# Optimization experiments

Measured on AMD Instinct MI355X. Metric: run time of the kernel, lower is better.

## Reference

```python
import jax, jax.numpy as jnp
import numpy as np

N_NODES = 200000
IN_DIM = 128
HID = 256
OUT = 128
B = 2048
K = 16  # sampled temporal fanout per hop


def setup_inputs() -> dict:
    rng = np.random.default_rng(0)
    x = rng.standard_normal((N_NODES, IN_DIM), dtype=np.float32)
    batch = rng.integers(0, N_NODES, size=B).astype(np.int32)
    ts = rng.uniform(0.5, 1.0, size=B).astype(np.float32)

    # hop 1: K temporal neighbors per seed node, edge times <= query time
    nbr1 = rng.integers(0, N_NODES, size=B * K).astype(np.int32)
    t_edge1 = (rng.uniform(0.0, 1.0, size=(B, K)) * ts[:, None]).astype(np.float32)
    n_times1 = t_edge1.max(axis=1)                       # [B] max neighbor time per seed
    seg1 = np.repeat(np.arange(B, dtype=np.int32), K)    # [E1]

    # second-level frontier: neighbors first, then the batch itself
    nodes2 = np.concatenate([nbr1, batch])               # [N2 = B*K + B]
    t2 = np.concatenate([t_edge1.reshape(-1), ts]).astype(np.float32)
    N2 = nodes2.shape[0]

    # hop 2
    nbr2 = rng.integers(0, N_NODES, size=N2 * K).astype(np.int32)
    t_edge2 = (rng.uniform(0.0, 1.0, size=(N2, K)) * t2[:, None]).astype(np.float32)
    n_times2 = t_edge2.max(axis=1)                       # [N2]
    seg2 = np.repeat(np.arange(N2, dtype=np.int32), K)   # [E2]

    def lin(ko, fan_out, fan_in):
        lim = 1.0 / np.sqrt(fan_in)
        kw, kb = jax.random.split(ko)
        W = jax.random.uniform(kw, (fan_out, fan_in), jnp.float32, -lim, lim)
        b = jax.random.uniform(kb, (fan_out,), jnp.float32, -lim, lim)
        return W, b

    key = jax.random.key(0)
    k1, k2, k3, k4, k5 = jax.random.split(key, 5)
    W1n, b1n = lin(k1, HID, IN_DIM)
    W1h, b1h = lin(k2, HID, IN_DIM)
    W2n, b2n = lin(k3, OUT, HID)
    W2h, b2h = lin(k4, OUT, HID)
    t_kernel = jax.random.uniform(k5, (1,), jnp.float32)

    return {
        "x": jnp.asarray(x), "ts": jnp.asarray(ts), "t2": jnp.asarray(t2),
        "n_times1": jnp.asarray(n_times1), "n_times2": jnp.asarray(n_times2),
        "W1n": W1n, "b1n": b1n, "W1h": W1h, "b1h": b1h,
        "W2n": W2n, "b2n": b2n, "W2h": W2h, "b2h": b2h,
        "t_kernel": t_kernel,
        "nodes2": jnp.asarray(nodes2), "nbr2": jnp.asarray(nbr2),
        "seg2": jnp.asarray(seg2), "seg1": jnp.asarray(seg1),
    }


def reference(x, ts, t2, n_times1, n_times2, W1n, b1n, W1h, b1h,
              W2n, b2n, W2h, b2h, t_kernel, nodes2, nbr2, seg2, seg1):
    N2 = nodes2.shape[0]
    Bn = ts.shape[0]
    E1 = N2 - Bn

    def decay(dt):  # exp(-t_kernel * dt), t_kernel shape (1,) broadcasts
        return jnp.exp(-t_kernel * dt)

    # ---- layer 1 (inner recursion; layer-0 embeddings are raw features x) ----
    agg2 = jax.ops.segment_sum(x[nbr2], seg2, num_segments=N2)   # [N2, D] neighbor sums
    hn1 = x[nodes2] * decay(t2 - n_times2)[:, None]              # self feats * temporal decay
    h1 = jax.nn.relu(agg2 @ W1n.T + b1n + hn1 @ W1h.T + b1h)     # [N2, HID]

    # ---- layer 2 (top) ----
    agg1 = jax.ops.segment_sum(h1[:E1], seg1, num_segments=Bn)   # [B, HID]
    hn2 = h1[E1:] * decay(ts - n_times1)[:, None]                # [B, HID]
    out = jax.nn.relu(agg1 @ W2n.T + b2n + hn2 @ W2h.T + b2h)    # [B, OUT]
    return out
```

## Files before the change

kernel.cpp:

```cpp
#include <hip/hip_runtime.h>
#include <hip/hip_bf16.h>

#define N2V    34816
#define BATCH  2048
#define E1V    32768
#define KFAN   16
#define INDIM  128
#define HID    256
#define OUTD   128

#define OFF_BS1   0
#define OFF_BS2   256
#define OFF_WC1B  384
#define OFF_WC2B  33152
#define OFF_AGG1B 65920
#define OFF_H1S   328064

typedef __attribute__((ext_vector_type(8))) short bf16x8;
typedef __attribute__((ext_vector_type(4))) short short4v;
typedef __attribute__((ext_vector_type(4))) float f32x4;

__device__ __forceinline__ float bf2f(short u) {
  union { unsigned u32; float f; } cv;
  cv.u32 = ((unsigned)(unsigned short)u) << 16;
  return cv.f;
}

__device__ __forceinline__ short f2b(float f) {
  __hip_bfloat16 h = __float2bfloat16(f);
  return *reinterpret_cast<short*>(&h);
}

__global__ __launch_bounds__(256) void prepack_kernel(
    const float* __restrict__ W1n, const float* __restrict__ b1n,
    const float* __restrict__ W1h, const float* __restrict__ b1h,
    const float* __restrict__ W2n, const float* __restrict__ b2n,
    const float* __restrict__ W2h, const float* __restrict__ b2h,
    __hip_bfloat16* __restrict__ Wc1b, __hip_bfloat16* __restrict__ Wc2b,
    float* __restrict__ bs1, float* __restrict__ bs2) {
  int idx = blockIdx.x * 256 + threadIdx.x;
  int j1 = idx >> 8, c1 = idx & 255;
  float v1 = (c1 < 128) ? W1n[j1 * 128 + c1] : W1h[j1 * 128 + (c1 - 128)];
  Wc1b[idx] = __float2bfloat16(v1);
  int j2 = idx >> 9, c2 = idx & 511;
  float v2 = (c2 < 256) ? W2n[j2 * 256 + c2] : W2h[j2 * 256 + (c2 - 256)];
  Wc2b[idx] = __float2bfloat16(v2);
  if (idx < 256) bs1[idx] = b1n[idx] + b1h[idx];
  if (idx < 128) bs2[idx] = b2n[idx] + b2h[idx];
}

__global__ __launch_bounds__(256) void fused1_kernel(
    const float* __restrict__ x, const float* __restrict__ t2,
    const float* __restrict__ n_times2, const int* __restrict__ nodes2,
    const int* __restrict__ nbr2, const float* __restrict__ tk,
    const __hip_bfloat16* __restrict__ Wc1b, const float* __restrict__ bs1,
    __hip_bfloat16* __restrict__ agg1b, __hip_bfloat16* __restrict__ h1s) {
  __shared__ __hip_bfloat16 z[16][264];
  const int t = threadIdx.x;
  const int i0 = blockIdx.x * 16;
  {
    const int r = t >> 4;
    const int c = t & 15;
    const int i = i0 + r;
    const float4* __restrict__ x4 = (const float4*)x;

    const int4* nb4 = reinterpret_cast<const int4*>(nbr2) + i * 4;
    int4 n0 = nb4[0], n1 = nb4[1], n2 = nb4[2], n3 = nb4[3];
    const int idx[16] = {n0.x, n0.y, n0.z, n0.w, n1.x, n1.y, n1.z, n1.w,
                         n2.x, n2.y, n2.z, n2.w, n3.x, n3.y, n3.z, n3.w};

    float4 s0 = {0.f, 0.f, 0.f, 0.f};
    float4 s1 = {0.f, 0.f, 0.f, 0.f};
#pragma unroll
    for (int k = 0; k < KFAN; ++k) {
      const float4* rp = x4 + (size_t)idx[k] * 32;
      float4 v0 = rp[c];
      float4 v1 = rp[16 + c];
      s0.x += v0.x; s0.y += v0.y; s0.z += v0.z; s0.w += v0.w;
      s1.x += v1.x; s1.y += v1.y; s1.z += v1.z; s1.w += v1.w;
    }
    const float dec = __expf(-tk[0] * (t2[i] - n_times2[i]));
    const float4* sp = x4 + (size_t)nodes2[i] * 32;
    float4 u0 = sp[c];
    float4 u1 = sp[16 + c];

    char* zrow = (char*)&z[0][0] + r * 528;
    short4v p;
    p = (short4v){f2b(s0.x), f2b(s0.y), f2b(s0.z), f2b(s0.w)};
    *reinterpret_cast<short4v*>(zrow + c * 8) = p;
    p = (short4v){f2b(s1.x), f2b(s1.y), f2b(s1.z), f2b(s1.w)};
    *reinterpret_cast<short4v*>(zrow + 128 + c * 8) = p;
    p = (short4v){f2b(u0.x * dec), f2b(u0.y * dec), f2b(u0.z * dec), f2b(u0.w * dec)};
    *reinterpret_cast<short4v*>(zrow + 256 + c * 8) = p;
    p = (short4v){f2b(u1.x * dec), f2b(u1.y * dec), f2b(u1.z * dec), f2b(u1.w * dec)};
    *reinterpret_cast<short4v*>(zrow + 384 + c * 8) = p;
  }
  __syncthreads();

  const int wid = t >> 6;
  const int lane = t & 63;
  const int lr = lane & 15;
  const int lk8 = (lane >> 4) * 8;
  const int ncol0 = wid * 64;
  const short* __restrict__ wsrc = (const short*)Wc1b;

  f32x4 acc[4];
#pragma unroll
  for (int n = 0; n < 4; ++n) acc[n] = (f32x4){0.f, 0.f, 0.f, 0.f};

#pragma unroll
  for (int ks = 0; ks < 8; ++ks) {
    const int kb = ks * 32 + lk8;
    bf16x8 a = *reinterpret_cast<const bf16x8*>((char*)&z[0][0] + lr * 528 + kb * 2);
#pragma unroll
    for (int nt = 0; nt < 4; ++nt) {
      bf16x8 b = *reinterpret_cast<const bf16x8*>(
          wsrc + (size_t)(ncol0 + nt * 16 + lr) * 256 + kb);
      acc[nt] = __builtin_amdgcn_mfma_f32_16x16x32_bf16(a, b, acc[nt], 0, 0, 0);
    }
  }

  if (i0 < E1V) {
#pragma unroll
    for (int nt = 0; nt < 4; ++nt) {
      const int col = ncol0 + nt * 16 + lr;
      const float bias = bs1[col];
      float v = 0.f;
#pragma unroll
      for (int q = 0; q < 4; ++q) v += fmaxf(acc[nt][q] + bias, 0.f);
      v += __shfl_xor(v, 16);
      v += __shfl_xor(v, 32);
      if (lane < 16) {
        agg1b[(size_t)blockIdx.x * HID + col] = __float2bfloat16(v);
      }
    }
  } else {
    const int orow = (lane >> 4) * 4;
#pragma unroll
    for (int nt = 0; nt < 4; ++nt) {
      const int col = ncol0 + nt * 16 + lr;
      const float bias = bs1[col];
#pragma unroll
      for (int q = 0; q < 4; ++q) {
        const int row = i0 - E1V + orow + q;
        h1s[(size_t)row * HID + col] =
            __float2bfloat16(fmaxf(acc[nt][q] + bias, 0.f));
      }
    }
  }
}

__global__ __launch_bounds__(64) void layer2_kernel(
    const __hip_bfloat16* __restrict__ agg1b, const __hip_bfloat16* __restrict__ h1s,
    const float* __restrict__ ts, const float* __restrict__ n_times1,
    const float* __restrict__ tk, const __hip_bfloat16* __restrict__ Wc2b,
    const float* __restrict__ bs2, float* __restrict__ out) {
  const int lane = threadIdx.x;
  const int b0 = blockIdx.x * 16;
  const int lr = lane & 15;
  const int lk8 = (lane >> 4) * 8;
  const int row = b0 + lr;

  const float dec = __expf(-tk[0] * (ts[row] - n_times1[row]));
  const short* __restrict__ ag = (const short*)agg1b;
  const short* __restrict__ hs = (const short*)h1s;
  const short* __restrict__ w2 = (const short*)Wc2b;

  f32x4 acc[8];
#pragma unroll
  for (int n = 0; n < 8; ++n) acc[n] = (f32x4){0.f, 0.f, 0.f, 0.f};

#pragma unroll
  for (int ks = 0; ks < 16; ++ks) {
    const int kb = ks * 32 + lk8;
    bf16x8 a;
    if (kb < HID) {
      a = *reinterpret_cast<const bf16x8*>(ag + (size_t)row * HID + kb);
    } else {
      bf16x8 hv = *reinterpret_cast<const bf16x8*>(hs + (size_t)row * HID + (kb - HID));
#pragma unroll
      for (int e = 0; e < 8; ++e) a[e] = f2b(bf2f(hv[e]) * dec);
    }
#pragma unroll
    for (int nt = 0; nt < 8; ++nt) {
      bf16x8 b = *reinterpret_cast<const bf16x8*>(
          w2 + (size_t)(nt * 16 + lr) * 512 + kb);
      acc[nt] = __builtin_amdgcn_mfma_f32_16x16x32_bf16(a, b, acc[nt], 0, 0, 0);
    }
  }

  const int orow = (lane >> 4) * 4;
#pragma unroll
  for (int nt = 0; nt < 8; ++nt) {
    const int col = nt * 16 + lr;
    const float bias = bs2[col];
#pragma unroll
    for (int q = 0; q < 4; ++q) {
      out[(size_t)(b0 + orow + q) * OUTD + col] = fmaxf(acc[nt][q] + bias, 0.f);
    }
  }
}

extern "C" void kernel_launch(void* const* d_in, const int* in_sizes, int n_in,
                              void* d_out, int out_size, void* d_ws, size_t ws_size,
                              hipStream_t stream) {
  const float* x        = (const float*)d_in[0];
  const float* ts       = (const float*)d_in[1];
  const float* t2       = (const float*)d_in[2];
  const float* n_times1 = (const float*)d_in[3];
  const float* n_times2 = (const float*)d_in[4];
  const float* W1n      = (const float*)d_in[5];
  const float* b1n      = (const float*)d_in[6];
  const float* W1h      = (const float*)d_in[7];
  const float* b1h      = (const float*)d_in[8];
  const float* W2n      = (const float*)d_in[9];
  const float* b2n      = (const float*)d_in[10];
  const float* W2h      = (const float*)d_in[11];
  const float* b2h      = (const float*)d_in[12];
  const float* tk       = (const float*)d_in[13];
  const int*   nodes2   = (const int*)d_in[14];
  const int*   nbr2     = (const int*)d_in[15];

  float* ws = (float*)d_ws;
  float* bs1 = ws + OFF_BS1;
  float* bs2 = ws + OFF_BS2;
  __hip_bfloat16* Wc1b  = (__hip_bfloat16*)(ws + OFF_WC1B);
  __hip_bfloat16* Wc2b  = (__hip_bfloat16*)(ws + OFF_WC2B);
  __hip_bfloat16* agg1b = (__hip_bfloat16*)(ws + OFF_AGG1B);
  __hip_bfloat16* h1s   = (__hip_bfloat16*)(ws + OFF_H1S);
  float* out = (float*)d_out;

  prepack_kernel<<<256, 256, 0, stream>>>(W1n, b1n, W1h, b1h,
                                          W2n, b2n, W2h, b2h,
                                          Wc1b, Wc2b, bs1, bs2);
  fused1_kernel<<<N2V / 16, 256, 0, stream>>>(x, t2, n_times2, nodes2, nbr2, tk,
                                              Wc1b, bs1, agg1b, h1s);
  layer2_kernel<<<BATCH / 16, 64, 0, stream>>>(agg1b, h1s, ts, n_times1, tk,
                                               Wc2b, bs2, out);
}
```

Measured before the change: 77.21 us.

## Process two row tiles per block, overlapping next tile's gather with current GEMM

Each fused1 block now handles two 16-row tiles with a double-buffered LDS staging area. The gather loads for the second tile (first half of the features plus the self row) are issued before the first tile's MFMA GEMM so memory latency can overlap compute, with explicit barriers and scheduling fences around it. The grid is halved and launch bounds request 3 blocks per CU. In exchange, register pressure rises (16 float4 values held across the GEMM), which could lower occupancy or cause spills, and halving the block count reduces parallelism for a gather-bound kernel.

```diff
diff --git a/kernel.cpp b/kernel.cpp
--- a/kernel.cpp
+++ b/kernel.cpp
@@ -8,6 +8,7 @@
 #define INDIM  128
 #define HID    256
 #define OUTD   128
+#define E1TILES (E1V / 16)
 
 #define OFF_BS1   0
 #define OFF_BS2   256
@@ -49,26 +50,86 @@
   if (idx < 128) bs2[idx] = b2n[idx] + b2h[idx];
 }
 
-__global__ __launch_bounds__(256) void fused1_kernel(
+__device__ __forceinline__ void gemm_tile(
+    const __hip_bfloat16* zb, int tile, int t,
+    const short* __restrict__ wsrc, const float* __restrict__ bs1,
+    __hip_bfloat16* __restrict__ agg1b, __hip_bfloat16* __restrict__ h1s) {
+  const int wid = t >> 6;
+  const int lane = t & 63;
+  const int lr = lane & 15;
+  const int lk8 = (lane >> 4) * 8;
+  const int ncol0 = wid * 64;
+
+  f32x4 acc[4];
+#pragma unroll
+  for (int n = 0; n < 4; ++n) acc[n] = (f32x4){0.f, 0.f, 0.f, 0.f};
+
+#pragma unroll
+  for (int ks = 0; ks < 8; ++ks) {
+    const int kb = ks * 32 + lk8;
+    bf16x8 a = *reinterpret_cast<const bf16x8*>(
+        (const char*)zb + lr * 528 + kb * 2);
+#pragma unroll
+    for (int nt = 0; nt < 4; ++nt) {
+      bf16x8 b = *reinterpret_cast<const bf16x8*>(
+          wsrc + (size_t)(ncol0 + nt * 16 + lr) * 256 + kb);
+      acc[nt] = __builtin_amdgcn_mfma_f32_16x16x32_bf16(a, b, acc[nt], 0, 0, 0);
+    }
+  }
+
+  if (tile < E1TILES) {
+#pragma unroll
+    for (int nt = 0; nt < 4; ++nt) {
+      const int col = ncol0 + nt * 16 + lr;
+      const float bias = bs1[col];
+      float v = 0.f;
+#pragma unroll
+      for (int q = 0; q < 4; ++q) v += fmaxf(acc[nt][q] + bias, 0.f);
+      v += __shfl_xor(v, 16);
+      v += __shfl_xor(v, 32);
+      if (lane < 16) {
+        agg1b[(size_t)tile * HID + col] = __float2bfloat16(v);
+      }
+    }
+  } else {
+    const int orow = (lane >> 4) * 4;
+    const int rbase = tile * 16 - E1V;
+#pragma unroll
+    for (int nt = 0; nt < 4; ++nt) {
+      const int col = ncol0 + nt * 16 + lr;
+      const float bias = bs1[col];
+#pragma unroll
+      for (int q = 0; q < 4; ++q) {
+        h1s[(size_t)(rbase + orow + q) * HID + col] =
+            __float2bfloat16(fmaxf(acc[nt][q] + bias, 0.f));
+      }
+    }
+  }
+}
+
+__global__ __launch_bounds__(256, 3) void fused1_kernel(
     const float* __restrict__ x, const float* __restrict__ t2,
     const float* __restrict__ n_times2, const int* __restrict__ nodes2,
     const int* __restrict__ nbr2, const float* __restrict__ tk,
     const __hip_bfloat16* __restrict__ Wc1b, const float* __restrict__ bs1,
     __hip_bfloat16* __restrict__ agg1b, __hip_bfloat16* __restrict__ h1s) {
-  __shared__ __hip_bfloat16 z[16][264];
+  __shared__ __hip_bfloat16 z[2][16][264];
   const int t = threadIdx.x;
-  const int i0 = blockIdx.x * 16;
+  const int r = t >> 4;
+  const int c = t & 15;
+  const int tileA = blockIdx.x * 2;
+  const int tileB = tileA + 1;
+  const int iA = tileA * 16 + r;
+  const int iB = tileB * 16 + r;
+  const float4* __restrict__ x4 = (const float4*)x;
+  const float tkv = tk[0];
+  const short* __restrict__ wsrc = (const short*)Wc1b;
+
   {
-    const int r = t >> 4;
-    const int c = t & 15;
-    const int i = i0 + r;
-    const float4* __restrict__ x4 = (const float4*)x;
-
-    const int4* nb4 = reinterpret_cast<const int4*>(nbr2) + i * 4;
+    const int4* nb4 = reinterpret_cast<const int4*>(nbr2) + iA * 4;
     int4 n0 = nb4[0], n1 = nb4[1], n2 = nb4[2], n3 = nb4[3];
     const int idx[16] = {n0.x, n0.y, n0.z, n0.w, n1.x, n1.y, n1.z, n1.w,
                          n2.x, n2.y, n2.z, n2.w, n3.x, n3.y, n3.z, n3.w};
-
     float4 s0 = {0.f, 0.f, 0.f, 0.f};
     float4 s1 = {0.f, 0.f, 0.f, 0.f};
 #pragma unroll
@@ -79,12 +140,12 @@
       s0.x += v0.x; s0.y += v0.y; s0.z += v0.z; s0.w += v0.w;
       s1.x += v1.x; s1.y += v1.y; s1.z += v1.z; s1.w += v1.w;
     }
-    const float dec = __expf(-tk[0] * (t2[i] - n_times2[i]));
-    const float4* sp = x4 + (size_t)nodes2[i] * 32;
+    const float dec = __expf(-tkv * (t2[iA] - n_times2[iA]));
+    const float4* sp = x4 + (size_t)nodes2[iA] * 32;
     float4 u0 = sp[c];
     float4 u1 = sp[16 + c];
 
-    char* zrow = (char*)&z[0][0] + r * 528;
+    char* zrow = (char*)&z[0][0][0] + r * 528;
     short4v p;
     p = (short4v){f2b(s0.x), f2b(s0.y), f2b(s0.z), f2b(s0.w)};
     *reinterpret_cast<short4v*>(zrow + c * 8) = p;
@@ -95,59 +156,61 @@
     p = (short4v){f2b(u1.x * dec), f2b(u1.y * dec), f2b(u1.z * dec), f2b(u1.w * dec)};
     *reinterpret_cast<short4v*>(zrow + 384 + c * 8) = p;
   }
-  __syncthreads();
-
-  const int wid = t >> 6;
-  const int lane = t & 63;
-  const int lr = lane & 15;
-  const int lk8 = (lane >> 4) * 8;
-  const int ncol0 = wid * 64;
-  const short* __restrict__ wsrc = (const short*)Wc1b;
-
-  f32x4 acc[4];
-#pragma unroll
-  for (int n = 0; n < 4; ++n) acc[n] = (f32x4){0.f, 0.f, 0.f, 0.f};
-
-#pragma unroll
-  for (int ks = 0; ks < 8; ++ks) {
-    const int kb = ks * 32 + lk8;
-    bf16x8 a = *reinterpret_cast<const bf16x8*>((char*)&z[0][0] + lr * 528 + kb * 2);
-#pragma unroll
-    for (int nt = 0; nt < 4; ++nt) {
-      bf16x8 b = *reinterpret_cast<const bf16x8*>(
-          wsrc + (size_t)(ncol0 + nt * 16 + lr) * 256 + kb);
-      acc[nt] = __builtin_amdgcn_mfma_f32_16x16x32_bf16(a, b, acc[nt], 0, 0, 0);
-    }
-  }
-
-  if (i0 < E1V) {
-#pragma unroll
-    for (int nt = 0; nt < 4; ++nt) {
-      const int col = ncol0 + nt * 16 + lr;
-      const float bias = bs1[col];
-      float v = 0.f;
-#pragma unroll
-      for (int q = 0; q < 4; ++q) v += fmaxf(acc[nt][q] + bias, 0.f);
-      v += __shfl_xor(v, 16);
-      v += __shfl_xor(v, 32);
-      if (lane < 16) {
-        agg1b[(size_t)blockIdx.x * HID + col] = __float2bfloat16(v);
-      }
-    }
-  } else {
-    const int orow = (lane >> 4) * 4;
-#pragma unroll
-    for (int nt = 0; nt < 4; ++nt) {
-      const int col = ncol0 + nt * 16 + lr;
-      const float bias = bs1[col];
-#pragma unroll
-      for (int q = 0; q < 4; ++q) {
-        const int row = i0 - E1V + orow + q;
-        h1s[(size_t)row * HID + col] =
-            __float2bfloat16(fmaxf(acc[nt][q] + bias, 0.f));
-      }
-    }
-  }
+
+  int idxB[16];
+  {
+    const int4* nb4 = reinterpret_cast<const int4*>(nbr2) + iB * 4;
+    int4 n0 = nb4[0], n1 = nb4[1], n2 = nb4[2], n3 = nb4[3];
+    idxB[0] = n0.x; idxB[1] = n0.y; idxB[2]  = n0.z; idxB[3]  = n0.w;
+    idxB[4] = n1.x; idxB[5] = n1.y; idxB[6]  = n1.z; idxB[7]  = n1.w;
+    idxB[8] = n2.x; idxB[9] = n2.y; idxB[10] = n2.z; idxB[11] = n2.w;
+    idxB[12] = n3.x; idxB[13] = n3.y; idxB[14] = n3.z; idxB[15] = n3.w;
+  }
+  float4 vB[16];
+#pragma unroll
+  for (int k = 0; k < KFAN; ++k)
+    vB[k] = x4[(size_t)idxB[k] * 32 + c];
+  const float4* spB = x4 + (size_t)nodes2[iB] * 32;
+  float4 uB0 = spB[c];
+  float4 uB1 = spB[16 + c];
+  const float decB = __expf(-tkv * (t2[iB] - n_times2[iB]));
+
+  asm volatile("s_waitcnt lgkmcnt(0)" ::: "memory");
+  __builtin_amdgcn_s_barrier();
+  __builtin_amdgcn_sched_barrier(0);
+
+  gemm_tile(&z[0][0][0], tileA, t, wsrc, bs1, agg1b, h1s);
+
+  {
+    float4 s0 = {0.f, 0.f, 0.f, 0.f};
+#pragma unroll
+    for (int k = 0; k < KFAN; ++k) {
+      s0.x += vB[k].x; s0.y += vB[k].y; s0.z += vB[k].z; s0.w += vB[k].w;
+    }
+    float4 s1 = {0.f, 0.f, 0.f, 0.f};
+#pragma unroll
+    for (int k = 0; k < KFAN; ++k) {
+      float4 v1 = x4[(size_t)idxB[k] * 32 + 16 + c];
+      s1.x += v1.x; s1.y += v1.y; s1.z += v1.z; s1.w += v1.w;
+    }
+
+    char* zrow = (char*)&z[1][0][0] + r * 528;
+    short4v p;
+    p = (short4v){f2b(s0.x), f2b(s0.y), f2b(s0.z), f2b(s0.w)};
+    *reinterpret_cast<short4v*>(zrow + c * 8) = p;
+    p = (short4v){f2b(s1.x), f2b(s1.y), f2b(s1.z), f2b(s1.w)};
+    *reinterpret_cast<short4v*>(zrow + 128 + c * 8) = p;
+    p = (short4v){f2b(uB0.x * decB), f2b(uB0.y * decB), f2b(uB0.z * decB), f2b(uB0.w * decB)};
+    *reinterpret_cast<short4v*>(zrow + 256 + c * 8) = p;
+    p = (short4v){f2b(uB1.x * decB), f2b(uB1.y * decB), f2b(uB1.z * decB), f2b(uB1.w * decB)};
+    *reinterpret_cast<short4v*>(zrow + 384 + c * 8) = p;
+  }
+
+  asm volatile("s_waitcnt lgkmcnt(0)" ::: "memory");
+  __builtin_amdgcn_s_barrier();
+  __builtin_amdgcn_sched_barrier(0);
+
+  gemm_tile(&z[1][0][0], tileB, t, wsrc, bs1, agg1b, h1s);
 }
 
 __global__ __launch_bounds__(64) void layer2_kernel(
@@ -233,7 +296,7 @@
   prepack_kernel<<<256, 256, 0, stream>>>(W1n, b1n, W1h, b1h,
                                           W2n, b2n, W2h, b2h,
                                           Wc1b, Wc2b, bs1, bs2);
-  fused1_kernel<<<N2V / 16, 256, 0, stream>>>(x, t2, n_times2, nodes2, nbr2, tk,
+  fused1_kernel<<<N2V / 32, 256, 0, stream>>>(x, t2, n_times2, nodes2, nbr2, tk,
                                               Wc1b, bs1, agg1b, h1s);
   layer2_kernel<<<BATCH / 16, 64, 0, stream>>>(agg1b, h1s, ts, n_times1, tk,
                                                Wc2b, bs2, out);
```

New measurement: 99.55 us. 28.9% more time.

## Warp-specialize fused layer-1 kernel into producer gather and consumer MFMA waves

Applied to the files above, without the earlier changes.

Each block now handles four 16-row tiles with 512 threads. The first 256 threads gather and aggregate neighbour features into a double-buffered LDS tile, while the other 256 threads run the MFMA GEMM and epilogue on the previous tile. The aim is to overlap the latency-bound random gathers of x with the matrix multiply and the output writes. The cost is a barrier per tile, a quarter as many blocks, and half of each block's threads sitting idle during the prologue and final tile.

```diff
diff --git a/kernel.cpp b/kernel.cpp
--- a/kernel.cpp
+++ b/kernel.cpp
@@ -8,6 +8,9 @@
 #define INDIM  128
 #define HID    256
 #define OUTD   128
+#define E1TILES (E1V / 16)
+#define TPB    4
+#define FUSED_BLOCKS (N2V / 16 / TPB)
 
 #define OFF_BS1   0
 #define OFF_BS2   256
@@ -49,103 +52,132 @@
   if (idx < 128) bs2[idx] = b2n[idx] + b2h[idx];
 }
 
-__global__ __launch_bounds__(256) void fused1_kernel(
+__device__ __forceinline__ void gather_tile(
+    int tile, int t, const float4* __restrict__ x4,
+    const float* __restrict__ t2, const float* __restrict__ n_times2,
+    const int* __restrict__ nodes2, const int* __restrict__ nbr2,
+    float tkv, __hip_bfloat16* zb) {
+  const int r = t >> 4;
+  const int c = t & 15;
+  const int i = tile * 16 + r;
+
+  const int4* nb4 = reinterpret_cast<const int4*>(nbr2) + i * 4;
+  int4 n0 = nb4[0], n1 = nb4[1], n2 = nb4[2], n3 = nb4[3];
+  const int idx[16] = {n0.x, n0.y, n0.z, n0.w, n1.x, n1.y, n1.z, n1.w,
+                       n2.x, n2.y, n2.z, n2.w, n3.x, n3.y, n3.z, n3.w};
+
+  float4 s0 = {0.f, 0.f, 0.f, 0.f};
+  float4 s1 = {0.f, 0.f, 0.f, 0.f};
+#pragma unroll
+  for (int k = 0; k < KFAN; ++k) {
+    const float4* rp = x4 + (size_t)idx[k] * 32;
+    float4 v0 = rp[c];
+    float4 v1 = rp[16 + c];
+    s0.x += v0.x; s0.y += v0.y; s0.z += v0.z; s0.w += v0.w;
+    s1.x += v1.x; s1.y += v1.y; s1.z += v1.z; s1.w += v1.w;
+  }
+  const float dec = __expf(-tkv * (t2[i] - n_times2[i]));
+  const float4* sp = x4 + (size_t)nodes2[i] * 32;
+  float4 u0 = sp[c];
+  float4 u1 = sp[16 + c];
+
+  char* zrow = (char*)zb + r * 528;
+  short4v p;
+  p = (short4v){f2b(s0.x), f2b(s0.y), f2b(s0.z), f2b(s0.w)};
+  *reinterpret_cast<short4v*>(zrow + c * 8) = p;
+  p = (short4v){f2b(s1.x), f2b(s1.y), f2b(s1.z), f2b(s1.w)};
+  *reinterpret_cast<short4v*>(zrow + 128 + c * 8) = p;
+  p = (short4v){f2b(u0.x * dec), f2b(u0.y * dec), f2b(u0.z * dec), f2b(u0.w * dec)};
+  *reinterpret_cast<short4v*>(zrow + 256 + c * 8) = p;
+  p = (short4v){f2b(u1.x * dec), f2b(u1.y * dec), f2b(u1.z * dec), f2b(u1.w * dec)};
+  *reinterpret_cast<short4v*>(zrow + 384 + c * 8) = p;
+}
+
+__device__ __forceinline__ void gemm_tile(
+    const __hip_bfloat16* zb, int tile, int tc,
+    const short* __restrict__ wsrc, const float* __restrict__ bs1,
+    __hip_bfloat16* __restrict__ agg1b, __hip_bfloat16* __restrict__ h1s) {
+  const int wid = tc >> 6;
+  const int lane = tc & 63;
+  const int lr = lane & 15;
+  const int lk8 = (lane >> 4) * 8;
+  const int ncol0 = wid * 64;
+
+  f32x4 acc[4];
+#pragma unroll
+  for (int n = 0; n < 4; ++n) acc[n] = (f32x4){0.f, 0.f, 0.f, 0.f};
+
+#pragma unroll
+  for (int ks = 0; ks < 8; ++ks) {
+    const int kb = ks * 32 + lk8;
+    bf16x8 a = *reinterpret_cast<const bf16x8*>(
+        (const char*)zb + lr * 528 + kb * 2);
+#pragma unroll
+    for (int nt = 0; nt < 4; ++nt) {
+      bf16x8 b = *reinterpret_cast<const bf16x8*>(
+          wsrc + (size_t)(ncol0 + nt * 16 + lr) * 256 + kb);
+      acc[nt] = __builtin_amdgcn_mfma_f32_16x16x32_bf16(a, b, acc[nt], 0, 0, 0);
+    }
+  }
+
+  if (tile < E1TILES) {
+#pragma unroll
+    for (int nt = 0; nt < 4; ++nt) {
+      const int col = ncol0 + nt * 16 + lr;
+      const float bias = bs1[col];
+      float v = 0.f;
+#pragma unroll
+      for (int q = 0; q < 4; ++q) v += fmaxf(acc[nt][q] + bias, 0.f);
+      v += __shfl_xor(v, 16);
+      v += __shfl_xor(v, 32);
+      if (lane < 16) {
+        agg1b[(size_t)tile * HID + col] = __float2bfloat16(v);
+      }
+    }
+  } else {
+    const int orow = (lane >> 4) * 4;
+    const int rbase = tile * 16 - E1V;
+#pragma unroll
+    for (int nt = 0; nt < 4; ++nt) {
+      const int col = ncol0 + nt * 16 + lr;
+      const float bias = bs1[col];
+#pragma unroll
+      for (int q = 0; q < 4; ++q) {
+        h1s[(size_t)(rbase + orow + q) * HID + col] =
+            __float2bfloat16(fmaxf(acc[nt][q] + bias, 0.f));
+      }
+    }
+  }
+}
+
+__global__ __launch_bounds__(512, 4) void fused1_kernel(
     const float* __restrict__ x, const float* __restrict__ t2,
     const float* __restrict__ n_times2, const int* __restrict__ nodes2,
     const int* __restrict__ nbr2, const float* __restrict__ tk,
     const __hip_bfloat16* __restrict__ Wc1b, const float* __restrict__ bs1,
     __hip_bfloat16* __restrict__ agg1b, __hip_bfloat16* __restrict__ h1s) {
-  __shared__ __hip_bfloat16 z[16][264];
+  __shared__ __hip_bfloat16 z[2][16][264];
   const int t = threadIdx.x;
-  const int i0 = blockIdx.x * 16;
-  {
-    const int r = t >> 4;
-    const int c = t & 15;
-    const int i = i0 + r;
-    const float4* __restrict__ x4 = (const float4*)x;
-
-    const int4* nb4 = reinterpret_cast<const int4*>(nbr2) + i * 4;
-    int4 n0 = nb4[0], n1 = nb4[1], n2 = nb4[2], n3 = nb4[3];
-    const int idx[16] = {n0.x, n0.y, n0.z, n0.w, n1.x, n1.y, n1.z, n1.w,
-                         n2.x, n2.y, n2.z, n2.w, n3.x, n3.y, n3.z, n3.w};
-
-    float4 s0 = {0.f, 0.f, 0.f, 0.f};
-    float4 s1 = {0.f, 0.f, 0.f, 0.f};
-#pragma unroll
-    for (int k = 0; k < KFAN; ++k) {
-      const float4* rp = x4 + (size_t)idx[k] * 32;
-      float4 v0 = rp[c];
-      float4 v1 = rp[16 + c];
-      s0.x += v0.x; s0.y += v0.y; s0.z += v0.z; s0.w += v0.w;
-      s1.x += v1.x; s1.y += v1.y; s1.z += v1.z; s1.w += v1.w;
-    }
-    const float dec = __expf(-tk[0] * (t2[i] - n_times2[i]));
-    const float4* sp = x4 + (size_t)nodes2[i] * 32;
-    float4 u0 = sp[c];
-    float4 u1 = sp[16 + c];
-
-    char* zrow = (char*)&z[0][0] + r * 528;
-    short4v p;
-    p = (short4v){f2b(s0.x), f2b(s0.y), f2b(s0.z), f2b(s0.w)};
-    *reinterpret_cast<short4v*>(zrow + c * 8) = p;
-    p = (short4v){f2b(s1.x), f2b(s1.y), f2b(s1.z), f2b(s1.w)};
-    *reinterpret_cast<short4v*>(zrow + 128 + c * 8) = p;
-    p = (short4v){f2b(u0.x * dec), f2b(u0.y * dec), f2b(u0.z * dec), f2b(u0.w * dec)};
-    *reinterpret_cast<short4v*>(zrow + 256 + c * 8) = p;
-    p = (short4v){f2b(u1.x * dec), f2b(u1.y * dec), f2b(u1.z * dec), f2b(u1.w * dec)};
-    *reinterpret_cast<short4v*>(zrow + 384 + c * 8) = p;
-  }
-  __syncthreads();
-
-  const int wid = t >> 6;
-  const int lane = t & 63;
-  const int lr = lane & 15;
-  const int lk8 = (lane >> 4) * 8;
-  const int ncol0 = wid * 64;
+  const int tile0 = blockIdx.x * TPB;
+  const float4* __restrict__ x4 = (const float4*)x;
   const short* __restrict__ wsrc = (const short*)Wc1b;
-
-  f32x4 acc[4];
-#pragma unroll
-  for (int n = 0; n < 4; ++n) acc[n] = (f32x4){0.f, 0.f, 0.f, 0.f};
-
-#pragma unroll
-  for (int ks = 0; ks < 8; ++ks) {
-    const int kb = ks * 32 + lk8;
-    bf16x8 a = *reinterpret_cast<const bf16x8*>((char*)&z[0][0] + lr * 528 + kb * 2);
-#pragma unroll
-    for (int nt = 0; nt < 4; ++nt) {
-      bf16x8 b = *reinterpret_cast<const bf16x8*>(
-          wsrc + (size_t)(ncol0 + nt * 16 + lr) * 256 + kb);
-      acc[nt] = __builtin_amdgcn_mfma_f32_16x16x32_bf16(a, b, acc[nt], 0, 0, 0);
-    }
-  }
-
-  if (i0 < E1V) {
-#pragma unroll
-    for (int nt = 0; nt < 4; ++nt) {
-      const int col = ncol0 + nt * 16 + lr;
-      const float bias = bs1[col];
-      float v = 0.f;
-#pragma unroll
-      for (int q = 0; q < 4; ++q) v += fmaxf(acc[nt][q] + bias, 0.f);
-      v += __shfl_xor(v, 16);
-      v += __shfl_xor(v, 32);
-      if (lane < 16) {
-        agg1b[(size_t)blockIdx.x * HID + col] = __float2bfloat16(v);
+  const float tkv = tk[0];
+  const bool producer = (t < 256);
+
+  if (producer) {
+    gather_tile(tile0, t, x4, t2, n_times2, nodes2, nbr2, tkv, &z[0][0][0]);
+  }
+
+#pragma unroll
+  for (int j = 0; j < TPB; ++j) {
+    __syncthreads();
+    if (producer) {
+      if (j + 1 < TPB) {
+        gather_tile(tile0 + j + 1, t, x4, t2, n_times2, nodes2, nbr2, tkv,
+                    &z[(j + 1) & 1][0][0]);
       }
-    }
-  } else {
-    const int orow = (lane >> 4) * 4;
-#pragma unroll
-    for (int nt = 0; nt < 4; ++nt) {
-      const int col = ncol0 + nt * 16 + lr;
-      const float bias = bs1[col];
-#pragma unroll
-      for (int q = 0; q < 4; ++q) {
-        const int row = i0 - E1V + orow + q;
-        h1s[(size_t)row * HID + col] =
-            __float2bfloat16(fmaxf(acc[nt][q] + bias, 0.f));
-      }
+    } else {
+      gemm_tile(&z[j & 1][0][0], tile0 + j, t - 256, wsrc, bs1, agg1b, h1s);
     }
   }
 }
@@ -233,8 +265,8 @@
   prepack_kernel<<<256, 256, 0, stream>>>(W1n, b1n, W1h, b1h,
                                           W2n, b2n, W2h, b2h,
                                           Wc1b, Wc2b, bs1, bs2);
-  fused1_kernel<<<N2V / 16, 256, 0, stream>>>(x, t2, n_times2, nodes2, nbr2, tk,
-                                              Wc1b, bs1, agg1b, h1s);
+  fused1_kernel<<<FUSED_BLOCKS, 512, 0, stream>>>(x, t2, n_times2, nodes2, nbr2,
+                                                  tk, Wc1b, bs1, agg1b, h1s);
   layer2_kernel<<<BATCH / 16, 64, 0, stream>>>(agg1b, h1s, ts, n_times1, tk,
                                                Wc2b, bs2, out);
 }
```

Measured after the change: 105.0 us (median of 3 runs). +36.0%, slower.
